# Performance work log

Hardware: AMD Instinct MI355X
Metric: run time of the kernel (lower is better)

## Reference

```python
import jax, jax.numpy as jnp
import numpy as np

V = 128000
SHORTLIST = 10  # cutoffs[0]


def _gru_cell(x, h, w_ih, w_hh, b_ih, b_hh):
    # PyTorch GRU cell math. x: [B, In], h: [B, H], w_*: [3H, *]
    gi = x @ w_ih.T + b_ih  # [B, 3H]
    gh = h @ w_hh.T + b_hh  # [B, 3H]
    i_r, i_z, i_n = jnp.split(gi, 3, axis=-1)
    h_r, h_z, h_n = jnp.split(gh, 3, axis=-1)
    r = jax.nn.sigmoid(i_r + h_r)
    z = jax.nn.sigmoid(i_z + h_z)
    n = jnp.tanh(i_n + r * h_n)
    return (1.0 - z) * n + z * h


def setup_inputs() -> dict:
    key = jax.random.key(0)
    ks = jax.random.split(key, 20)
    B, E, H = 256, 512, 1024
    s = 0.02
    return {
        "input": jax.random.randint(ks[0], (B,), 0, V),
        "hidden": jax.random.normal(ks[1], (2, B, H), jnp.float32),
        "start_state": jnp.zeros((2, B, H), jnp.float32),
        "emb": jax.random.normal(ks[2], (V, E), jnp.float32) * s,
        "w_ih0": jax.random.normal(ks[3], (3 * H, E), jnp.float32) * s,
        "w_hh0": jax.random.normal(ks[4], (3 * H, H), jnp.float32) * s,
        "b_ih0": jax.random.normal(ks[5], (3 * H,), jnp.float32) * s,
        "b_hh0": jax.random.normal(ks[6], (3 * H,), jnp.float32) * s,
        "w_ih1": jax.random.normal(ks[7], (3 * H, H), jnp.float32) * s,
        "w_hh1": jax.random.normal(ks[8], (3 * H, H), jnp.float32) * s,
        "b_ih1": jax.random.normal(ks[9], (3 * H,), jnp.float32) * s,
        "b_hh1": jax.random.normal(ks[10], (3 * H,), jnp.float32) * s,
        "head_w": jax.random.normal(ks[11], (12, H), jnp.float32) * s,
        "t0_proj": jax.random.normal(ks[12], (256, H), jnp.float32) * s,
        "t0_out": jax.random.normal(ks[13], (2, 256), jnp.float32) * s,
        "t1_proj": jax.random.normal(ks[14], (64, H), jnp.float32) * s,
        "t1_out": jax.random.normal(ks[15], (V - 12, 64), jnp.float32) * s,
    }


def reference(input, hidden, start_state, emb, w_ih0, w_hh0, b_ih0, b_hh0,
              w_ih1, w_hh1, b_ih1, b_hh1, head_w, t0_proj, t0_out, t1_proj, t1_out):
    # Embedding lookup (seq_len = 1, squeezed away)
    x = emb[input]  # [B, E]
    # Stacked single-step GRU (eval mode: no dropout)
    h0 = _gru_cell(x, hidden[0], w_ih0, w_hh0, b_ih0, b_hh0)
    h1 = _gru_cell(h0, hidden[1], w_ih1, w_hh1, b_ih1, b_hh1)
    new_hidden = jnp.stack([h0, h1], axis=0)
    out = h1  # [B, H]
    # AdaptiveLogSoftmax.log_prob: head + two tail clusters
    head_lp = jax.nn.log_softmax(out @ head_w.T, axis=-1)  # [B, 12]
    c0 = jax.nn.log_softmax((out @ t0_proj.T) @ t0_out.T, axis=-1)  # [B, 2]
    c1 = jax.nn.log_softmax((out @ t1_proj.T) @ t1_out.T, axis=-1)  # [B, V-12]
    prediction = jnp.concatenate([
        head_lp[:, :SHORTLIST],
        c0 + head_lp[:, SHORTLIST:SHORTLIST + 1],
        c1 + head_lp[:, SHORTLIST + 1:SHORTLIST + 2],
    ], axis=-1)  # [B, V]
    return prediction, new_hidden
```

## Files before the change

kernel.cpp:

```cpp
#include <hip/hip_runtime.h>
#include <hip/hip_bf16.h>
#include <math.h>


#define BM 64
#define BN 64
#define BK 32

typedef __attribute__((ext_vector_type(8))) short frag_ab;
typedef __attribute__((ext_vector_type(4))) float frag_cd;
typedef __attribute__((ext_vector_type(4))) float floatx4;

__device__ __forceinline__ unsigned short f2bf(float f) {
    unsigned int u = __builtin_bit_cast(unsigned int, f);
    u += 0x7fffu + ((u >> 16) & 1u);
    return (unsigned short)(u >> 16);
}

__global__ __launch_bounds__(256) void gru_gemm(const int* __restrict__ idx,
                                                const float* __restrict__ A_ih,
                                                const float* __restrict__ A_hh,
                                                const float* __restrict__ W_ih,
                                                const float* __restrict__ W_hh,
                                                float* __restrict__ outbase,
                                                int Kih, int Khh) {
    const int z = blockIdx.z;
    const int side = z >> 1, half = z & 1;
    const int K = side ? Khh : Kih;
    const int Kh = K >> 1;
    const float* A = side ? A_hh : A_ih;
    const float* W = side ? W_hh : W_ih;
    float* C = outbase + (size_t)z * 786432;

    __shared__ unsigned short As[BM * BK];
    __shared__ unsigned short Wsh[BN * BK];
    const int m0 = blockIdx.y * BM, n0 = blockIdx.x * BN;
    const int t = threadIdx.x;
    const int lane = t & 63, wid = t >> 6;
    const int wm = wid >> 1, wn = wid & 1;
    const int quad = lane >> 4, l16 = lane & 15;
    const int lr = t >> 2;
    const int lc = (t & 3) * 8;

    const int m = m0 + lr;
    const float* arow = (side == 0 && idx) ? A + (size_t)idx[m] * K
                                           : A + (size_t)m * K;
    arow += (size_t)half * Kh + lc;
    const float* wrow = W + (size_t)(n0 + lr) * K + (size_t)half * Kh + lc;

    frag_cd zero4 = {0.f, 0.f, 0.f, 0.f};
    frag_cd acc[2][2] = {{zero4, zero4}, {zero4, zero4}};

    for (int k0 = 0; k0 < Kh; k0 += BK) {
        floatx4 a0 = *(const floatx4*)(arow + k0);
        floatx4 a1 = *(const floatx4*)(arow + k0 + 4);
        floatx4 w0 = *(const floatx4*)(wrow + k0);
        floatx4 w1 = *(const floatx4*)(wrow + k0 + 4);
        frag_ab apk, wpk;
#pragma unroll
        for (int i = 0; i < 4; i++) {
            apk[i]     = (short)f2bf(a0[i]);
            apk[4 + i] = (short)f2bf(a1[i]);
            wpk[i]     = (short)f2bf(w0[i]);
            wpk[4 + i] = (short)f2bf(w1[i]);
        }
        __syncthreads();
        *(frag_ab*)&As[lr * BK + lc] = apk;
        *(frag_ab*)&Wsh[lr * BK + lc] = wpk;
        __syncthreads();

        frag_ab bfr[2];
#pragma unroll
        for (int tn = 0; tn < 2; tn++)
            bfr[tn] = *(const frag_ab*)&Wsh[(wn * 32 + tn * 16 + l16) * BK + quad * 8];
#pragma unroll
        for (int tm = 0; tm < 2; tm++) {
            frag_ab af = *(const frag_ab*)&As[(wm * 32 + tm * 16 + l16) * BK + quad * 8];
#pragma unroll
            for (int tn = 0; tn < 2; tn++)
                acc[tm][tn] = __builtin_amdgcn_mfma_f32_16x16x32_bf16(af, bfr[tn], acc[tm][tn], 0, 0, 0);
        }
    }
#pragma unroll
    for (int tm = 0; tm < 2; tm++)
#pragma unroll
        for (int tn = 0; tn < 2; tn++) {
            int col = n0 + wn * 32 + tn * 16 + l16;
#pragma unroll
            for (int r = 0; r < 4; r++) {
                int row = m0 + wm * 32 + tm * 16 + quad * 4 + r;
                C[(size_t)row * 3072 + col] = acc[tm][tn][r];
            }
        }
}

__global__ __launch_bounds__(256) void gru_gate(const float* __restrict__ P,
                                                const float* __restrict__ b_ih,
                                                const float* __restrict__ b_hh,
                                                const float* __restrict__ hprev,
                                                float* __restrict__ hout) {
    int idx = blockIdx.x * 256 + threadIdx.x;
    int b = idx >> 10, j = idx & 1023;
    const float* g = P + (size_t)b * 3072 + j;
    float ir  = g[0]    + g[786432]        + b_ih[j];
    float iz  = g[1024] + g[786432 + 1024] + b_ih[1024 + j];
    float in_ = g[2048] + g[786432 + 2048] + b_ih[2048 + j];
    const float* gh = g + 2 * 786432;
    float hr  = gh[0]    + gh[786432]        + b_hh[j];
    float hz  = gh[1024] + gh[786432 + 1024] + b_hh[1024 + j];
    float hn  = gh[2048] + gh[786432 + 2048] + b_hh[2048 + j];
    float r = 1.f / (1.f + __expf(-(ir + hr)));
    float z = 1.f / (1.f + __expf(-(iz + hz)));
    float n = tanhf(in_ + r * hn);
    hout[idx] = (1.f - z) * n + z * hprev[idx];
}

__global__ __launch_bounds__(256) void small_gemm(const float* __restrict__ A,
                                                  const float* __restrict__ head_w,
                                                  const float* __restrict__ t0_proj,
                                                  const float* __restrict__ t1_proj,
                                                  float* __restrict__ c_p) {
    const int K = 1024, Kh = 512;
    const int half = blockIdx.z;
    float* C = c_p + (size_t)half * 98304;

    __shared__ unsigned short As[BM * BK];
    __shared__ unsigned short Wsh[BN * BK];
    const int m0 = blockIdx.y * BM, n0 = blockIdx.x * BN;
    const int t = threadIdx.x;
    const int lane = t & 63, wid = t >> 6;
    const int wm = wid >> 1, wn = wid & 1;
    const int quad = lane >> 4, l16 = lane & 15;
    const int lr = t >> 2;
    const int lc = (t & 3) * 8;

    const float* arow = A + (size_t)(m0 + lr) * K + (size_t)half * Kh + lc;
    int wr = n0 + lr;
    const float* wrow;
    if (wr < 12)       wrow = head_w  + (size_t)wr * K;
    else if (wr < 268) wrow = t0_proj + (size_t)(wr - 12) * K;
    else if (wr < 332) wrow = t1_proj + (size_t)(wr - 268) * K;
    else               wrow = nullptr;
    if (wrow) wrow += (size_t)half * Kh + lc;

    frag_cd zero4 = {0.f, 0.f, 0.f, 0.f};
    frag_cd acc[2][2] = {{zero4, zero4}, {zero4, zero4}};

    for (int k0 = 0; k0 < Kh; k0 += BK) {
        floatx4 a0 = *(const floatx4*)(arow + k0);
        floatx4 a1 = *(const floatx4*)(arow + k0 + 4);
        floatx4 w0 = {0.f, 0.f, 0.f, 0.f}, w1 = {0.f, 0.f, 0.f, 0.f};
        if (wrow) {
            w0 = *(const floatx4*)(wrow + k0);
            w1 = *(const floatx4*)(wrow + k0 + 4);
        }
        frag_ab apk, wpk;
#pragma unroll
        for (int i = 0; i < 4; i++) {
            apk[i]     = (short)f2bf(a0[i]);
            apk[4 + i] = (short)f2bf(a1[i]);
            wpk[i]     = (short)f2bf(w0[i]);
            wpk[4 + i] = (short)f2bf(w1[i]);
        }
        __syncthreads();
        *(frag_ab*)&As[lr * BK + lc] = apk;
        *(frag_ab*)&Wsh[lr * BK + lc] = wpk;
        __syncthreads();

        frag_ab bfr[2];
#pragma unroll
        for (int tn = 0; tn < 2; tn++)
            bfr[tn] = *(const frag_ab*)&Wsh[(wn * 32 + tn * 16 + l16) * BK + quad * 8];
#pragma unroll
        for (int tm = 0; tm < 2; tm++) {
            frag_ab af = *(const frag_ab*)&As[(wm * 32 + tm * 16 + l16) * BK + quad * 8];
#pragma unroll
            for (int tn = 0; tn < 2; tn++)
                acc[tm][tn] = __builtin_amdgcn_mfma_f32_16x16x32_bf16(af, bfr[tn], acc[tm][tn], 0, 0, 0);
        }
    }
#pragma unroll
    for (int tm = 0; tm < 2; tm++)
#pragma unroll
        for (int tn = 0; tn < 2; tn++) {
            int col = n0 + wn * 32 + tn * 16 + l16;
#pragma unroll
            for (int r = 0; r < 4; r++) {
                int row = m0 + wm * 32 + tm * 16 + quad * 4 + r;
                C[(size_t)row * 384 + col] = acc[tm][tn][r];
            }
        }
}

__global__ __launch_bounds__(256) void postproc(const float* __restrict__ c_p,
                                                const float* __restrict__ t0_out,
                                                float* __restrict__ outp,
                                                float* __restrict__ abuf,
                                                float* __restrict__ h11buf) {
    int b = blockIdx.x, t = threadIdx.x;
    __shared__ float c[332];
    __shared__ float a0s[4], a1s[4];
    __shared__ float sh_lse;
    for (int j = t; j < 332; j += 256)
        c[j] = c_p[(size_t)b * 384 + j] + c_p[98304 + (size_t)b * 384 + j];
    __syncthreads();
    if (t == 0) {
        float m = c[0];
        for (int i = 1; i < 12; i++) m = fmaxf(m, c[i]);
        float se = 0.f;
        for (int i = 0; i < 12; i++) se += __expf(c[i] - m);
        sh_lse = m + logf(se);
    }
    __syncthreads();
    if (t < 10) outp[(size_t)b * 128000 + t] = c[t] - sh_lse;
    if (t < 64) abuf[(size_t)b * 64 + t] = c[268 + t];

    float pv = c[12 + t];
    float s0 = pv * t0_out[t];
    float s1 = pv * t0_out[256 + t];
    s0 += __shfl_xor(s0, 1);  s0 += __shfl_xor(s0, 2);  s0 += __shfl_xor(s0, 4);
    s0 += __shfl_xor(s0, 8);  s0 += __shfl_xor(s0, 16); s0 += __shfl_xor(s0, 32);
    s1 += __shfl_xor(s1, 1);  s1 += __shfl_xor(s1, 2);  s1 += __shfl_xor(s1, 4);
    s1 += __shfl_xor(s1, 8);  s1 += __shfl_xor(s1, 16); s1 += __shfl_xor(s1, 32);
    if ((t & 63) == 0) { a0s[t >> 6] = s0; a1s[t >> 6] = s1; }
    __syncthreads();
    if (t == 0) {
        float l0 = a0s[0] + a0s[1] + a0s[2] + a0s[3];
        float l1 = a1s[0] + a1s[1] + a1s[2] + a1s[3];
        float m = fmaxf(l0, l1);
        float lse2 = m + logf(__expf(l0 - m) + __expf(l1 - m));
        float hp = c[10] - sh_lse;
        outp[(size_t)b * 128000 + 10] = l0 - lse2 + hp;
        outp[(size_t)b * 128000 + 11] = l1 - lse2 + hp;
        h11buf[b] = c[11] - sh_lse;
    }
}

__global__ __launch_bounds__(256) void big_pass1(const float* __restrict__ A,
                                                 const float* __restrict__ W,
                                                 float* __restrict__ partials) {
    const int N = 127988, K = 64;
    __shared__ unsigned short As[BM * BK];
    __shared__ unsigned short Wsh[BN * BK];
    __shared__ float rowsum[BM];
    const int m0 = blockIdx.y * BM, n0 = blockIdx.x * BN;
    const int t = threadIdx.x;
    const int lane = t & 63, wid = t >> 6;
    const int wm = wid >> 1, wn = wid & 1;
    const int quad = lane >> 4, l16 = lane & 15;
    const int lr = t >> 2;
    const int lc = (t & 3) * 8;

    if (t < BM) rowsum[t] = 0.f;

    const float* arow = A + (size_t)(m0 + lr) * K + lc;
    int wr = n0 + lr;
    const float* wrow = (wr < N) ? W + (size_t)wr * K + lc : nullptr;

    frag_cd zero4 = {0.f, 0.f, 0.f, 0.f};
    frag_cd acc[2][2] = {{zero4, zero4}, {zero4, zero4}};

    for (int k0 = 0; k0 < K; k0 += BK) {
        floatx4 a0 = *(const floatx4*)(arow + k0);
        floatx4 a1 = *(const floatx4*)(arow + k0 + 4);
        floatx4 w0 = {0.f, 0.f, 0.f, 0.f}, w1 = {0.f, 0.f, 0.f, 0.f};
        if (wrow) {
            w0 = *(const floatx4*)(wrow + k0);
            w1 = *(const floatx4*)(wrow + k0 + 4);
        }
        frag_ab apk, wpk;
#pragma unroll
        for (int i = 0; i < 4; i++) {
            apk[i]     = (short)f2bf(a0[i]);
            apk[4 + i] = (short)f2bf(a1[i]);
            wpk[i]     = (short)f2bf(w0[i]);
            wpk[4 + i] = (short)f2bf(w1[i]);
        }
        __syncthreads();
        *(frag_ab*)&As[lr * BK + lc] = apk;
        *(frag_ab*)&Wsh[lr * BK + lc] = wpk;
        __syncthreads();

        frag_ab bfr[2];
#pragma unroll
        for (int tn = 0; tn < 2; tn++)
            bfr[tn] = *(const frag_ab*)&Wsh[(wn * 32 + tn * 16 + l16) * BK + quad * 8];
#pragma unroll
        for (int tm = 0; tm < 2; tm++) {
            frag_ab af = *(const frag_ab*)&As[(wm * 32 + tm * 16 + l16) * BK + quad * 8];
#pragma unroll
            for (int tn = 0; tn < 2; tn++)
                acc[tm][tn] = __builtin_amdgcn_mfma_f32_16x16x32_bf16(af, bfr[tn], acc[tm][tn], 0, 0, 0);
        }
    }

#pragma unroll
    for (int tm = 0; tm < 2; tm++) {
#pragma unroll
        for (int r = 0; r < 4; r++) {
            float s = 0.f;
#pragma unroll
            for (int tn = 0; tn < 2; tn++) {
                int col = n0 + wn * 32 + tn * 16 + l16;
                if (col < N) s += __expf(acc[tm][tn][r]);
            }
            s += __shfl_xor(s, 1);
            s += __shfl_xor(s, 2);
            s += __shfl_xor(s, 4);
            s += __shfl_xor(s, 8);
            if (l16 == 0) atomicAdd(&rowsum[wm * 32 + tm * 16 + quad * 4 + r], s);
        }
    }
    __syncthreads();
    if (t < BM) partials[(size_t)(m0 + t) * 2048 + blockIdx.x] = rowsum[t];
}

__global__ __launch_bounds__(256) void reduce_kernel(const float* __restrict__ partials,
                                                     const float* __restrict__ h11buf,
                                                     float* __restrict__ rowOff) {
    int b = blockIdx.x, t = threadIdx.x;
    __shared__ float a[4];
    float s = 0.f;
    for (int k = t; k < 2000; k += 256) s += partials[(size_t)b * 2048 + k];
    s += __shfl_xor(s, 1);  s += __shfl_xor(s, 2);  s += __shfl_xor(s, 4);
    s += __shfl_xor(s, 8);  s += __shfl_xor(s, 16); s += __shfl_xor(s, 32);
    if ((t & 63) == 0) a[t >> 6] = s;
    __syncthreads();
    if (t == 0) rowOff[b] = h11buf[b] - logf(a[0] + a[1] + a[2] + a[3]);
}

__global__ __launch_bounds__(256) void big_pass2(const float* __restrict__ A,
                                                 const float* __restrict__ W,
                                                 const float* __restrict__ rowOff,
                                                 float* __restrict__ outp) {
    const int N = 127988, K = 64;
    __shared__ unsigned short As[BM * BK];
    __shared__ unsigned short Wsh[BN * BK];
    __shared__ float ro[BM];
    const int m0 = blockIdx.y * BM, n0 = blockIdx.x * BN;
    const int t = threadIdx.x;
    const int lane = t & 63, wid = t >> 6;
    const int wm = wid >> 1, wn = wid & 1;
    const int quad = lane >> 4, l16 = lane & 15;
    const int lr = t >> 2;
    const int lc = (t & 3) * 8;

    if (t < BM) ro[t] = rowOff[m0 + t];

    const float* arow = A + (size_t)(m0 + lr) * K + lc;
    int wr = n0 + lr;
    const float* wrow = (wr < N) ? W + (size_t)wr * K + lc : nullptr;

    frag_cd zero4 = {0.f, 0.f, 0.f, 0.f};
    frag_cd acc[2][2] = {{zero4, zero4}, {zero4, zero4}};

    for (int k0 = 0; k0 < K; k0 += BK) {
        floatx4 a0 = *(const floatx4*)(arow + k0);
        floatx4 a1 = *(const floatx4*)(arow + k0 + 4);
        floatx4 w0 = {0.f, 0.f, 0.f, 0.f}, w1 = {0.f, 0.f, 0.f, 0.f};
        if (wrow) {
            w0 = *(const floatx4*)(wrow + k0);
            w1 = *(const floatx4*)(wrow + k0 + 4);
        }
        frag_ab apk, wpk;
#pragma unroll
        for (int i = 0; i < 4; i++) {
            apk[i]     = (short)f2bf(a0[i]);
            apk[4 + i] = (short)f2bf(a1[i]);
            wpk[i]     = (short)f2bf(w0[i]);
            wpk[4 + i] = (short)f2bf(w1[i]);
        }
        __syncthreads();
        *(frag_ab*)&As[lr * BK + lc] = apk;
        *(frag_ab*)&Wsh[lr * BK + lc] = wpk;
        __syncthreads();

        frag_ab bfr[2];
#pragma unroll
        for (int tn = 0; tn < 2; tn++)
            bfr[tn] = *(const frag_ab*)&Wsh[(wn * 32 + tn * 16 + l16) * BK + quad * 8];
#pragma unroll
        for (int tm = 0; tm < 2; tm++) {
            frag_ab af = *(const frag_ab*)&As[(wm * 32 + tm * 16 + l16) * BK + quad * 8];
#pragma unroll
            for (int tn = 0; tn < 2; tn++)
                acc[tm][tn] = __builtin_amdgcn_mfma_f32_16x16x32_bf16(af, bfr[tn], acc[tm][tn], 0, 0, 0);
        }
    }

#pragma unroll
    for (int tm = 0; tm < 2; tm++)
#pragma unroll
        for (int tn = 0; tn < 2; tn++) {
            int col = n0 + wn * 32 + tn * 16 + l16;
            if (col < N) {
#pragma unroll
                for (int r = 0; r < 4; r++) {
                    int rl = wm * 32 + tm * 16 + quad * 4 + r;
                    outp[(size_t)(m0 + rl) * 128000 + 12 + col] = acc[tm][tn][r] + ro[rl];
                }
            }
        }
}

extern "C" void kernel_launch(void* const* d_in, const int* in_sizes, int n_in,
                              void* d_out, int out_size, void* d_ws, size_t ws_size,
                              hipStream_t stream) {
    const int*   input  = (const int*)d_in[0];
    const float* hidden = (const float*)d_in[1];
    const float* emb    = (const float*)d_in[3];
    const float* w_ih0  = (const float*)d_in[4];
    const float* w_hh0  = (const float*)d_in[5];
    const float* b_ih0  = (const float*)d_in[6];
    const float* b_hh0  = (const float*)d_in[7];
    const float* w_ih1  = (const float*)d_in[8];
    const float* w_hh1  = (const float*)d_in[9];
    const float* b_ih1  = (const float*)d_in[10];
    const float* b_hh1  = (const float*)d_in[11];
    const float* head_w = (const float*)d_in[12];
    const float* t0_proj = (const float*)d_in[13];
    const float* t0_out  = (const float*)d_in[14];
    const float* t1_proj = (const float*)d_in[15];
    const float* t1_out  = (const float*)d_in[16];

    float* outp = (float*)d_out;
    float* ws   = (float*)d_ws;

    float* gruws    = ws;
    float* c_p      = gruws + 4 * 786432;
    float* abuf     = c_p + 2 * 98304;
    float* h11buf   = abuf + 16384;
    float* rowOff   = h11buf + 256;
    float* partials = rowOff + 256;

    float* h0 = outp + 32768000;
    float* h1 = h0 + 262144;

    gru_gemm<<<dim3(48, 4, 4), 256, 0, stream>>>(input, emb, hidden,
                                                 w_ih0, w_hh0, gruws, 512, 1024);
    gru_gate<<<1024, 256, 0, stream>>>(gruws, b_ih0, b_hh0, hidden, h0);
    gru_gemm<<<dim3(48, 4, 4), 256, 0, stream>>>(nullptr, h0, hidden + 262144,
                                                 w_ih1, w_hh1, gruws, 1024, 1024);
    gru_gate<<<1024, 256, 0, stream>>>(gruws, b_ih1, b_hh1, hidden + 262144, h1);
    small_gemm<<<dim3(6, 4, 2), 256, 0, stream>>>(h1, head_w, t0_proj, t1_proj, c_p);
    postproc<<<256, 256, 0, stream>>>(c_p, t0_out, outp, abuf, h11buf);
    big_pass1<<<dim3(2000, 4), 256, 0, stream>>>(abuf, t1_out, partials);
    reduce_kernel<<<256, 256, 0, stream>>>(partials, h11buf, rowOff);
    big_pass2<<<dim3(2000, 4), 256, 0, stream>>>(abuf, t1_out, rowOff, outp);
}
```

Baseline: 519.6 us.

## Pre-convert operands to bf16 and restructure GEMMs to load MFMA fragments directly

New measurement: 577.2 us. 1.11x slower.

```diff
diff --git a/kernel.cpp b/kernel.cpp
--- a/kernel.cpp
+++ b/kernel.cpp
@@ -1,15 +1,11 @@
 #include <hip/hip_runtime.h>
-#include <hip/hip_bf16.h>
 #include <math.h>
 
-
-#define BM 64
-#define BN 64
-#define BK 32
 
 typedef __attribute__((ext_vector_type(8))) short frag_ab;
 typedef __attribute__((ext_vector_type(4))) float frag_cd;
 typedef __attribute__((ext_vector_type(4))) float floatx4;
+typedef __attribute__((ext_vector_type(4))) unsigned short ushortx4;
 
 __device__ __forceinline__ unsigned short f2bf(float f) {
     unsigned int u = __builtin_bit_cast(unsigned int, f);
@@ -17,69 +13,102 @@
     return (unsigned short)(u >> 16);
 }
 
-__global__ __launch_bounds__(256) void gru_gemm(const int* __restrict__ idx,
-                                                const float* __restrict__ A_ih,
-                                                const float* __restrict__ A_hh,
-                                                const float* __restrict__ W_ih,
-                                                const float* __restrict__ W_hh,
+#define XB_OFF      0u
+#define HB0_OFF     131072u
+#define HB1_OFF     393216u
+#define H0B_OFF     655360u
+#define H1B_OFF     917504u
+#define ABUF_OFF    1179648u
+#define WIH0_OFF    1196032u
+#define WHH0_OFF    2768896u
+#define WIH1_OFF    5914624u
+#define WHH1_OFF    9060352u
+#define WSM_OFF     12206080u
+#define WT1_OFF     12599296u
+
+__global__ __launch_bounds__(256) void prep(const int* __restrict__ idx,
+                                            const float* __restrict__ emb,
+                                            const float* __restrict__ hidden,
+                                            const float* __restrict__ w_ih0,
+                                            const float* __restrict__ w_hh0,
+                                            const float* __restrict__ w_ih1,
+                                            const float* __restrict__ w_hh1,
+                                            const float* __restrict__ head_w,
+                                            const float* __restrict__ t0_proj,
+                                            const float* __restrict__ t1_proj,
+                                            unsigned short* __restrict__ dst) {
+    for (int i = blockIdx.x * 256 + threadIdx.x; i < 3014656; i += gridDim.x * 256) {
+        const float* src;
+        unsigned short* d;
+        if (i < 1179648) {
+            if (i < 393216) { src = w_ih0 + (size_t)i * 4; d = dst + WIH0_OFF + (size_t)i * 4; }
+            else { int j = i - 393216; src = w_hh0 + (size_t)j * 4; d = dst + WHH0_OFF + (size_t)j * 4; }
+        } else if (i < 2752512) {
+            if (i < 1966080) { int j = i - 1179648; src = w_ih1 + (size_t)j * 4; d = dst + WIH1_OFF + (size_t)j * 4; }
+            else { int j = i - 1966080; src = w_hh1 + (size_t)j * 4; d = dst + WHH1_OFF + (size_t)j * 4; }
+        } else if (i < 2850816) {
+            int j = i - 2752512;
+            int row = j >> 8, cv = (j & 255) * 4;
+            d = dst + WSM_OFF + (size_t)j * 4;
+            if (row < 12)       src = head_w + (size_t)row * 1024 + cv;
+            else if (row < 268) src = t0_proj + (size_t)(row - 12) * 1024 + cv;
+            else if (row < 332) src = t1_proj + (size_t)(row - 268) * 1024 + cv;
+            else                src = nullptr;
+        } else if (i < 2883584) {
+            int j = i - 2850816;
+            int b = j >> 7, cv = (j & 127) * 4;
+            src = emb + (size_t)idx[b] * 512 + cv;
+            d = dst + XB_OFF + (size_t)j * 4;
+        } else if (i < 2949120) {
+            int j = i - 2883584; src = hidden + (size_t)j * 4; d = dst + HB0_OFF + (size_t)j * 4;
+        } else {
+            int j = i - 2949120; src = hidden + 262144 + (size_t)j * 4; d = dst + HB1_OFF + (size_t)j * 4;
+        }
+        floatx4 v = {0.f, 0.f, 0.f, 0.f};
+        if (src) v = *(const floatx4*)src;
+        ushortx4 o;
+        o[0] = f2bf(v[0]); o[1] = f2bf(v[1]); o[2] = f2bf(v[2]); o[3] = f2bf(v[3]);
+        *(ushortx4*)d = o;
+    }
+}
+
+__global__ __launch_bounds__(256) void gru_gemm(const unsigned short* __restrict__ A_ih,
+                                                const unsigned short* __restrict__ A_hh,
+                                                const unsigned short* __restrict__ W_ih,
+                                                const unsigned short* __restrict__ W_hh,
                                                 float* __restrict__ outbase,
                                                 int Kih, int Khh) {
     const int z = blockIdx.z;
     const int side = z >> 1, half = z & 1;
     const int K = side ? Khh : Kih;
     const int Kh = K >> 1;
-    const float* A = side ? A_hh : A_ih;
-    const float* W = side ? W_hh : W_ih;
+    const unsigned short* A = side ? A_hh : A_ih;
+    const unsigned short* W = side ? W_hh : W_ih;
     float* C = outbase + (size_t)z * 786432;
 
-    __shared__ unsigned short As[BM * BK];
-    __shared__ unsigned short Wsh[BN * BK];
-    const int m0 = blockIdx.y * BM, n0 = blockIdx.x * BN;
+    const int m0 = blockIdx.y * 64, n0 = blockIdx.x * 64;
     const int t = threadIdx.x;
     const int lane = t & 63, wid = t >> 6;
     const int wm = wid >> 1, wn = wid & 1;
     const int quad = lane >> 4, l16 = lane & 15;
-    const int lr = t >> 2;
-    const int lc = (t & 3) * 8;
-
-    const int m = m0 + lr;
-    const float* arow = (side == 0 && idx) ? A + (size_t)idx[m] * K
-                                           : A + (size_t)m * K;
-    arow += (size_t)half * Kh + lc;
-    const float* wrow = W + (size_t)(n0 + lr) * K + (size_t)half * Kh + lc;
+
+    const unsigned short* ap0 = A + (size_t)(m0 + wm * 32 + l16) * K + half * Kh + quad * 8;
+    const unsigned short* ap1 = ap0 + (size_t)16 * K;
+    const unsigned short* bp0 = W + (size_t)(n0 + wn * 32 + l16) * K + half * Kh + quad * 8;
+    const unsigned short* bp1 = bp0 + (size_t)16 * K;
 
     frag_cd zero4 = {0.f, 0.f, 0.f, 0.f};
     frag_cd acc[2][2] = {{zero4, zero4}, {zero4, zero4}};
-
-    for (int k0 = 0; k0 < Kh; k0 += BK) {
-        floatx4 a0 = *(const floatx4*)(arow + k0);
-        floatx4 a1 = *(const floatx4*)(arow + k0 + 4);
-        floatx4 w0 = *(const floatx4*)(wrow + k0);
-        floatx4 w1 = *(const floatx4*)(wrow + k0 + 4);
-        frag_ab apk, wpk;
-#pragma unroll
-        for (int i = 0; i < 4; i++) {
-            apk[i]     = (short)f2bf(a0[i]);
-            apk[4 + i] = (short)f2bf(a1[i]);
-            wpk[i]     = (short)f2bf(w0[i]);
-            wpk[4 + i] = (short)f2bf(w1[i]);
-        }
-        __syncthreads();
-        *(frag_ab*)&As[lr * BK + lc] = apk;
-        *(frag_ab*)&Wsh[lr * BK + lc] = wpk;
-        __syncthreads();
-
-        frag_ab bfr[2];
-#pragma unroll
-        for (int tn = 0; tn < 2; tn++)
-            bfr[tn] = *(const frag_ab*)&Wsh[(wn * 32 + tn * 16 + l16) * BK + quad * 8];
-#pragma unroll
-        for (int tm = 0; tm < 2; tm++) {
-            frag_ab af = *(const frag_ab*)&As[(wm * 32 + tm * 16 + l16) * BK + quad * 8];
-#pragma unroll
-            for (int tn = 0; tn < 2; tn++)
-                acc[tm][tn] = __builtin_amdgcn_mfma_f32_16x16x32_bf16(af, bfr[tn], acc[tm][tn], 0, 0, 0);
-        }
+#pragma unroll 4
+    for (int k0 = 0; k0 < Kh; k0 += 32) {
+        frag_ab a0 = *(const frag_ab*)(ap0 + k0);
+        frag_ab a1 = *(const frag_ab*)(ap1 + k0);
+        frag_ab b0 = *(const frag_ab*)(bp0 + k0);
+        frag_ab b1 = *(const frag_ab*)(bp1 + k0);
+        acc[0][0] = __builtin_amdgcn_mfma_f32_16x16x32_bf16(a0, b0, acc[0][0], 0, 0, 0);
+        acc[0][1] = __builtin_amdgcn_mfma_f32_16x16x32_bf16(a0, b1, acc[0][1], 0, 0, 0);
+        acc[1][0] = __builtin_amdgcn_mfma_f32_16x16x32_bf16(a1, b0, acc[1][0], 0, 0, 0);
+        acc[1][1] = __builtin_amdgcn_mfma_f32_16x16x32_bf16(a1, b1, acc[1][1], 0, 0, 0);
     }
 #pragma unroll
     for (int tm = 0; tm < 2; tm++)
@@ -98,7 +127,8 @@
                                                 const float* __restrict__ b_ih,
                                                 const float* __restrict__ b_hh,
                                                 const float* __restrict__ hprev,
-                                                float* __restrict__ hout) {
+                                                float* __restrict__ hout,
+                                                unsigned short* __restrict__ hb) {
     int idx = blockIdx.x * 256 + threadIdx.x;
     int b = idx >> 10, j = idx & 1023;
     const float* g = P + (size_t)b * 3072 + j;
@@ -112,72 +142,41 @@
     float r = 1.f / (1.f + __expf(-(ir + hr)));
     float z = 1.f / (1.f + __expf(-(iz + hz)));
     float n = tanhf(in_ + r * hn);
-    hout[idx] = (1.f - z) * n + z * hprev[idx];
-}
-
-__global__ __launch_bounds__(256) void small_gemm(const float* __restrict__ A,
-                                                  const float* __restrict__ head_w,
-                                                  const float* __restrict__ t0_proj,
-                                                  const float* __restrict__ t1_proj,
+    float v = (1.f - z) * n + z * hprev[idx];
+    hout[idx] = v;
+    hb[idx] = f2bf(v);
+}
+
+__global__ __launch_bounds__(256) void small_gemm(const unsigned short* __restrict__ A,
+                                                  const unsigned short* __restrict__ Wsm,
                                                   float* __restrict__ c_p) {
     const int K = 1024, Kh = 512;
     const int half = blockIdx.z;
     float* C = c_p + (size_t)half * 98304;
 
-    __shared__ unsigned short As[BM * BK];
-    __shared__ unsigned short Wsh[BN * BK];
-    const int m0 = blockIdx.y * BM, n0 = blockIdx.x * BN;
+    const int m0 = blockIdx.y * 64, n0 = blockIdx.x * 64;
     const int t = threadIdx.x;
     const int lane = t & 63, wid = t >> 6;
     const int wm = wid >> 1, wn = wid & 1;
     const int quad = lane >> 4, l16 = lane & 15;
-    const int lr = t >> 2;
-    const int lc = (t & 3) * 8;
-
-    const float* arow = A + (size_t)(m0 + lr) * K + (size_t)half * Kh + lc;
-    int wr = n0 + lr;
-    const float* wrow;
-    if (wr < 12)       wrow = head_w  + (size_t)wr * K;
-    else if (wr < 268) wrow = t0_proj + (size_t)(wr - 12) * K;
-    else if (wr < 332) wrow = t1_proj + (size_t)(wr - 268) * K;
-    else               wrow = nullptr;
-    if (wrow) wrow += (size_t)half * Kh + lc;
+
+    const unsigned short* ap0 = A + (size_t)(m0 + wm * 32 + l16) * K + half * Kh + quad * 8;
+    const unsigned short* ap1 = ap0 + (size_t)16 * K;
+    const unsigned short* bp0 = Wsm + (size_t)(n0 + wn * 32 + l16) * K + half * Kh + quad * 8;
+    const unsigned short* bp1 = bp0 + (size_t)16 * K;
 
     frag_cd zero4 = {0.f, 0.f, 0.f, 0.f};
     frag_cd acc[2][2] = {{zero4, zero4}, {zero4, zero4}};
-
-    for (int k0 = 0; k0 < Kh; k0 += BK) {
-        floatx4 a0 = *(const floatx4*)(arow + k0);
-        floatx4 a1 = *(const floatx4*)(arow + k0 + 4);
-        floatx4 w0 = {0.f, 0.f, 0.f, 0.f}, w1 = {0.f, 0.f, 0.f, 0.f};
-        if (wrow) {
-            w0 = *(const floatx4*)(wrow + k0);
-            w1 = *(const floatx4*)(wrow + k0 + 4);
-        }
-        frag_ab apk, wpk;
-#pragma unroll
-        for (int i = 0; i < 4; i++) {
-            apk[i]     = (short)f2bf(a0[i]);
-            apk[4 + i] = (short)f2bf(a1[i]);
-            wpk[i]     = (short)f2bf(w0[i]);
-            wpk[4 + i] = (short)f2bf(w1[i]);
-        }
-        __syncthreads();
-        *(frag_ab*)&As[lr * BK + lc] = apk;
-        *(frag_ab*)&Wsh[lr * BK + lc] = wpk;
-        __syncthreads();
-
-        frag_ab bfr[2];
-#pragma unroll
-        for (int tn = 0; tn < 2; tn++)
-            bfr[tn] = *(const frag_ab*)&Wsh[(wn * 32 + tn * 16 + l16) * BK + quad * 8];
-#pragma unroll
-        for (int tm = 0; tm < 2; tm++) {
-            frag_ab af = *(const frag_ab*)&As[(wm * 32 + tm * 16 + l16) * BK + quad * 8];
-#pragma unroll
-            for (int tn = 0; tn < 2; tn++)
-                acc[tm][tn] = __builtin_amdgcn_mfma_f32_16x16x32_bf16(af, bfr[tn], acc[tm][tn], 0, 0, 0);
-        }
+#pragma unroll 4
+    for (int k0 = 0; k0 < Kh; k0 += 32) {
+        frag_ab a0 = *(const frag_ab*)(ap0 + k0);
+        frag_ab a1 = *(const frag_ab*)(ap1 + k0);
+        frag_ab b0 = *(const frag_ab*)(bp0 + k0);
+        frag_ab b1 = *(const frag_ab*)(bp1 + k0);
+        acc[0][0] = __builtin_amdgcn_mfma_f32_16x16x32_bf16(a0, b0, acc[0][0], 0, 0, 0);
+        acc[0][1] = __builtin_amdgcn_mfma_f32_16x16x32_bf16(a0, b1, acc[0][1], 0, 0, 0);
+        acc[1][0] = __builtin_amdgcn_mfma_f32_16x16x32_bf16(a1, b0, acc[1][0], 0, 0, 0);
+        acc[1][1] = __builtin_amdgcn_mfma_f32_16x16x32_bf16(a1, b1, acc[1][1], 0, 0, 0);
     }
 #pragma unroll
     for (int tm = 0; tm < 2; tm++)
@@ -195,7 +194,7 @@
 __global__ __launch_bounds__(256) void postproc(const float* __restrict__ c_p,
                                                 const float* __restrict__ t0_out,
                                                 float* __restrict__ outp,
-                                                float* __restrict__ abuf,
+                                                unsigned short* __restrict__ abuf,
                                                 float* __restrict__ h11buf) {
     int b = blockIdx.x, t = threadIdx.x;
     __shared__ float c[332];
@@ -213,7 +212,7 @@
     }
     __syncthreads();
     if (t < 10) outp[(size_t)b * 128000 + t] = c[t] - sh_lse;
-    if (t < 64) abuf[(size_t)b * 64 + t] = c[268 + t];
+    if (t < 64) abuf[(size_t)b * 64 + t] = f2bf(c[268 + t]);
 
     float pv = c[12 + t];
     float s0 = pv * t0_out[t];
@@ -236,83 +235,72 @@
     }
 }
 
-__global__ __launch_bounds__(256) void big_pass1(const float* __restrict__ A,
+__global__ __launch_bounds__(256) void big_pass1(const unsigned short* __restrict__ Ab,
                                                  const float* __restrict__ W,
+                                                 unsigned short* __restrict__ Wb,
                                                  float* __restrict__ partials) {
-    const int N = 127988, K = 64;
-    __shared__ unsigned short As[BM * BK];
-    __shared__ unsigned short Wsh[BN * BK];
-    __shared__ float rowsum[BM];
-    const int m0 = blockIdx.y * BM, n0 = blockIdx.x * BN;
+    const int N = 127988;
     const int t = threadIdx.x;
     const int lane = t & 63, wid = t >> 6;
-    const int wm = wid >> 1, wn = wid & 1;
     const int quad = lane >> 4, l16 = lane & 15;
-    const int lr = t >> 2;
-    const int lc = (t & 3) * 8;
-
-    if (t < BM) rowsum[t] = 0.f;
-
-    const float* arow = A + (size_t)(m0 + lr) * K + lc;
-    int wr = n0 + lr;
-    const float* wrow = (wr < N) ? W + (size_t)wr * K + lc : nullptr;
-
-    frag_cd zero4 = {0.f, 0.f, 0.f, 0.f};
-    frag_cd acc[2][2] = {{zero4, zero4}, {zero4, zero4}};
-
-    for (int k0 = 0; k0 < K; k0 += BK) {
-        floatx4 a0 = *(const floatx4*)(arow + k0);
-        floatx4 a1 = *(const floatx4*)(arow + k0 + 4);
-        floatx4 w0 = {0.f, 0.f, 0.f, 0.f}, w1 = {0.f, 0.f, 0.f, 0.f};
-        if (wrow) {
-            w0 = *(const floatx4*)(wrow + k0);
-            w1 = *(const floatx4*)(wrow + k0 + 4);
-        }
-        frag_ab apk, wpk;
-#pragma unroll
-        for (int i = 0; i < 4; i++) {
-            apk[i]     = (short)f2bf(a0[i]);
-            apk[4 + i] = (short)f2bf(a1[i]);
-            wpk[i]     = (short)f2bf(w0[i]);
-            wpk[4 + i] = (short)f2bf(w1[i]);
-        }
-        __syncthreads();
-        *(frag_ab*)&As[lr * BK + lc] = apk;
-        *(frag_ab*)&Wsh[lr * BK + lc] = wpk;
-        __syncthreads();
-
-        frag_ab bfr[2];
-#pragma unroll
-        for (int tn = 0; tn < 2; tn++)
-            bfr[tn] = *(const frag_ab*)&Wsh[(wn * 32 + tn * 16 + l16) * BK + quad * 8];
-#pragma unroll
-        for (int tm = 0; tm < 2; tm++) {
-            frag_ab af = *(const frag_ab*)&As[(wm * 32 + tm * 16 + l16) * BK + quad * 8];
-#pragma unroll
-            for (int tn = 0; tn < 2; tn++)
-                acc[tm][tn] = __builtin_amdgcn_mfma_f32_16x16x32_bf16(af, bfr[tn], acc[tm][tn], 0, 0, 0);
-        }
-    }
-
-#pragma unroll
-    for (int tm = 0; tm < 2; tm++) {
+
+    frag_ab a[4][2];
+#pragma unroll
+    for (int mf = 0; mf < 4; mf++)
+#pragma unroll
+        for (int kf = 0; kf < 2; kf++)
+            a[mf][kf] = *(const frag_ab*)(Ab + (size_t)(wid * 64 + mf * 16 + l16) * 64 + kf * 32 + quad * 8);
+
+    float rs[4][4] = {};
+    for (int tt = 0; tt < 4; tt++) {
+        const int n0 = (blockIdx.x * 4 + tt) * 16;
+        const int nr = n0 + l16;
+        frag_ab bw0 = {0, 0, 0, 0, 0, 0, 0, 0};
+        frag_ab bw1 = {0, 0, 0, 0, 0, 0, 0, 0};
+        if (nr < N) {
+            const float* wp = W + (size_t)nr * 64 + quad * 8;
+            floatx4 w0 = *(const floatx4*)wp;
+            floatx4 w1 = *(const floatx4*)(wp + 4);
+            floatx4 w2 = *(const floatx4*)(wp + 32);
+            floatx4 w3 = *(const floatx4*)(wp + 36);
+#pragma unroll
+            for (int i = 0; i < 4; i++) {
+                bw0[i]     = (short)f2bf(w0[i]);
+                bw0[4 + i] = (short)f2bf(w1[i]);
+                bw1[i]     = (short)f2bf(w2[i]);
+                bw1[4 + i] = (short)f2bf(w3[i]);
+            }
+        }
+        if (wid == 0) {
+            unsigned short* wd = Wb + (size_t)nr * 64 + quad * 8;
+            *(frag_ab*)wd = bw0;
+            *(frag_ab*)(wd + 32) = bw1;
+        }
+        frag_cd zero4 = {0.f, 0.f, 0.f, 0.f};
+        frag_cd acc[4] = {zero4, zero4, zero4, zero4};
+#pragma unroll
+        for (int mf = 0; mf < 4; mf++) {
+            acc[mf] = __builtin_amdgcn_mfma_f32_16x16x32_bf16(a[mf][0], bw0, acc[mf], 0, 0, 0);
+            acc[mf] = __builtin_amdgcn_mfma_f32_16x16x32_bf16(a[mf][1], bw1, acc[mf], 0, 0, 0);
+        }
+        if (nr < N) {
+#pragma unroll
+            for (int mf = 0; mf < 4; mf++)
+#pragma unroll
+                for (int r = 0; r < 4; r++)
+                    rs[mf][r] += __expf(acc[mf][r]);
+        }
+    }
+#pragma unroll
+    for (int mf = 0; mf < 4; mf++)
 #pragma unroll
         for (int r = 0; r < 4; r++) {
-            float s = 0.f;
-#pragma unroll
-            for (int tn = 0; tn < 2; tn++) {
-                int col = n0 + wn * 32 + tn * 16 + l16;
-                if (col < N) s += __expf(acc[tm][tn][r]);
-            }
-            s += __shfl_xor(s, 1);
-            s += __shfl_xor(s, 2);
-            s += __shfl_xor(s, 4);
-            s += __shfl_xor(s, 8);
-            if (l16 == 0) atomicAdd(&rowsum[wm * 32 + tm * 16 + quad * 4 + r], s);
-        }
-    }
-    __syncthreads();
-    if (t < BM) partials[(size_t)(m0 + t) * 2048 + blockIdx.x] = rowsum[t];
+            float s = rs[mf][r];
+            s += __shfl_xor(s, 1); s += __shfl_xor(s, 2);
+            s += __shfl_xor(s, 4); s += __shfl_xor(s, 8);
+            if (l16 == 0)
+                partials[(size_t)(wid * 64 + mf * 16 + quad * 4 + r) * 2048 + blockIdx.x] = s;
+        }
 }
 
 __global__ __launch_bounds__(256) void reduce_kernel(const float* __restrict__ partials,
@@ -329,78 +317,51 @@
     if (t == 0) rowOff[b] = h11buf[b] - logf(a[0] + a[1] + a[2] + a[3]);
 }
 
-__global__ __launch_bounds__(256) void big_pass2(const float* __restrict__ A,
-                                                 const float* __restrict__ W,
+__global__ __launch_bounds__(256) void big_pass2(const unsigned short* __restrict__ Ab,
+                                                 const unsigned short* __restrict__ Wb,
                                                  const float* __restrict__ rowOff,
                                                  float* __restrict__ outp) {
-    const int N = 127988, K = 64;
-    __shared__ unsigned short As[BM * BK];
-    __shared__ unsigned short Wsh[BN * BK];
-    __shared__ float ro[BM];
-    const int m0 = blockIdx.y * BM, n0 = blockIdx.x * BN;
+    const int N = 127988;
     const int t = threadIdx.x;
     const int lane = t & 63, wid = t >> 6;
-    const int wm = wid >> 1, wn = wid & 1;
     const int quad = lane >> 4, l16 = lane & 15;
-    const int lr = t >> 2;
-    const int lc = (t & 3) * 8;
-
-    if (t < BM) ro[t] = rowOff[m0 + t];
-
-    const float* arow = A + (size_t)(m0 + lr) * K + lc;
-    int wr = n0 + lr;
-    const float* wrow = (wr < N) ? W + (size_t)wr * K + lc : nullptr;
-
-    frag_cd zero4 = {0.f, 0.f, 0.f, 0.f};
-    frag_cd acc[2][2] = {{zero4, zero4}, {zero4, zero4}};
-
-    for (int k0 = 0; k0 < K; k0 += BK) {
-        floatx4 a0 = *(const floatx4*)(arow + k0);
-        floatx4 a1 = *(const floatx4*)(arow + k0 + 4);
-        floatx4 w0 = {0.f, 0.f, 0.f, 0.f}, w1 = {0.f, 0.f, 0.f, 0.f};
-        if (wrow) {
-            w0 = *(const floatx4*)(wrow + k0);
-            w1 = *(const floatx4*)(wrow + k0 + 4);
-        }
-        frag_ab apk, wpk;
-#pragma unroll
-        for (int i = 0; i < 4; i++) {
-            apk[i]     = (short)f2bf(a0[i]);
-            apk[4 + i] = (short)f2bf(a1[i]);
-            wpk[i]     = (short)f2bf(w0[i]);
-            wpk[4 + i] = (short)f2bf(w1[i]);
-        }
-        __syncthreads();
-        *(frag_ab*)&As[lr * BK + lc] = apk;
-        *(frag_ab*)&Wsh[lr * BK + lc] = wpk;
-        __syncthreads();
-
-        frag_ab bfr[2];
-#pragma unroll
-        for (int tn = 0; tn < 2; tn++)
-            bfr[tn] = *(const frag_ab*)&Wsh[(wn * 32 + tn * 16 + l16) * BK + quad * 8];
-#pragma unroll
-        for (int tm = 0; tm < 2; tm++) {
-            frag_ab af = *(const frag_ab*)&As[(wm * 32 + tm * 16 + l16) * BK + quad * 8];
-#pragma unroll
-            for (int tn = 0; tn < 2; tn++)
-                acc[tm][tn] = __builtin_amdgcn_mfma_f32_16x16x32_bf16(af, bfr[tn], acc[tm][tn], 0, 0, 0);
-        }
-    }
-
-#pragma unroll
-    for (int tm = 0; tm < 2; tm++)
-#pragma unroll
-        for (int tn = 0; tn < 2; tn++) {
-            int col = n0 + wn * 32 + tn * 16 + l16;
-            if (col < N) {
-#pragma unroll
-                for (int r = 0; r < 4; r++) {
-                    int rl = wm * 32 + tm * 16 + quad * 4 + r;
-                    outp[(size_t)(m0 + rl) * 128000 + 12 + col] = acc[tm][tn][r] + ro[rl];
-                }
-            }
-        }
+
+    frag_ab a[4][2];
+#pragma unroll
+    for (int mf = 0; mf < 4; mf++)
+#pragma unroll
+        for (int kf = 0; kf < 2; kf++)
+            a[mf][kf] = *(const frag_ab*)(Ab + (size_t)(wid * 64 + mf * 16 + l16) * 64 + kf * 32 + quad * 8);
+
+    float ro[4][4];
+#pragma unroll
+    for (int mf = 0; mf < 4; mf++)
+#pragma unroll
+        for (int r = 0; r < 4; r++)
+            ro[mf][r] = rowOff[wid * 64 + mf * 16 + quad * 4 + r];
+
+    for (int tt = 0; tt < 4; tt++) {
+        const int n0 = (blockIdx.x * 4 + tt) * 16;
+        const int nr = n0 + l16;
+        const unsigned short* wp = Wb + (size_t)nr * 64 + quad * 8;
+        frag_ab bw0 = *(const frag_ab*)wp;
+        frag_ab bw1 = *(const frag_ab*)(wp + 32);
+        frag_cd zero4 = {0.f, 0.f, 0.f, 0.f};
+        frag_cd acc[4] = {zero4, zero4, zero4, zero4};
+#pragma unroll
+        for (int mf = 0; mf < 4; mf++) {
+            acc[mf] = __builtin_amdgcn_mfma_f32_16x16x32_bf16(a[mf][0], bw0, acc[mf], 0, 0, 0);
+            acc[mf] = __builtin_amdgcn_mfma_f32_16x16x32_bf16(a[mf][1], bw1, acc[mf], 0, 0, 0);
+        }
+        if (nr < N) {
+#pragma unroll
+            for (int mf = 0; mf < 4; mf++)
+#pragma unroll
+                for (int r = 0; r < 4; r++)
+                    outp[(size_t)(wid * 64 + mf * 16 + quad * 4 + r) * 128000 + 12 + nr] =
+                        acc[mf][r] + ro[mf][r];
+        }
+    }
 }
 
 extern "C" void kernel_launch(void* const* d_in, const int* in_sizes, int n_in,
@@ -427,24 +388,37 @@
     float* ws   = (float*)d_ws;
 
     float* gruws    = ws;
-    float* c_p      = gruws + 4 * 786432;
-    float* abuf     = c_p + 2 * 98304;
-    float* h11buf   = abuf + 16384;
+    float* c_p      = gruws + 3145728;
+    float* partials = c_p + 196608;
+    float* h11buf   = partials + 524288;
     float* rowOff   = h11buf + 256;
-    float* partials = rowOff + 256;
+    unsigned short* us = (unsigned short*)(rowOff + 256);
+
+    unsigned short* xb    = us + XB_OFF;
+    unsigned short* hb0   = us + HB0_OFF;
+    unsigned short* hb1   = us + HB1_OFF;
+    unsigned short* h0b   = us + H0B_OFF;
+    unsigned short* h1b   = us + H1B_OFF;
+    unsigned short* abufb = us + ABUF_OFF;
+    unsigned short* wih0  = us + WIH0_OFF;
+    unsigned short* whh0  = us + WHH0_OFF;
+    unsigned short* wih1  = us + WIH1_OFF;
+    unsigned short* whh1  = us + WHH1_OFF;
+    unsigned short* wsm   = us + WSM_OFF;
+    unsigned short* wt1   = us + WT1_OFF;
 
     float* h0 = outp + 32768000;
     float* h1 = h0 + 262144;
 
-    gru_gemm<<<dim3(48, 4, 4), 256, 0, stream>>>(input, emb, hidden,
-                                                 w_ih0, w_hh0, gruws, 512, 1024);
-    gru_gate<<<1024, 256, 0, stream>>>(gruws, b_ih0, b_hh0, hidden, h0);
-    gru_gemm<<<dim3(48, 4, 4), 256, 0, stream>>>(nullptr, h0, hidden + 262144,
-                                                 w_ih1, w_hh1, gruws, 1024, 1024);
-    gru_gate<<<1024, 256, 0, stream>>>(gruws, b_ih1, b_hh1, hidden + 262144, h1);
-    small_gemm<<<dim3(6, 4, 2), 256, 0, stream>>>(h1, head_w, t0_proj, t1_proj, c_p);
-    postproc<<<256, 256, 0, stream>>>(c_p, t0_out, outp, abuf, h11buf);
-    big_pass1<<<dim3(2000, 4), 256, 0, stream>>>(abuf, t1_out, partials);
+    prep<<<2048, 256, 0, stream>>>(input, emb, hidden, w_ih0, w_hh0, w_ih1, w_hh1,
+                                   head_w, t0_proj, t1_proj, us);
+    gru_gemm<<<dim3(48, 4, 4), 256, 0, stream>>>(xb, hb0, wih0, whh0, gruws, 512, 1024);
+    gru_gate<<<1024, 256, 0, stream>>>(gruws, b_ih0, b_hh0, hidden, h0, h0b);
+    gru_gemm<<<dim3(48, 4, 4), 256, 0, stream>>>(h0b, hb1, wih1, whh1, gruws, 1024, 1024);
+    gru_gate<<<1024, 256, 0, stream>>>(gruws, b_ih1, b_hh1, hidden + 262144, h1, h1b);
+    small_gemm<<<dim3(6, 4, 2), 256, 0, stream>>>(h1b, wsm, c_p);
+    postproc<<<256, 256, 0, stream>>>(c_p, t0_out, outp, abufb, h11buf);
+    big_pass1<<<2000, 256, 0, stream>>>(abufb, t1_out, wt1, partials);
     reduce_kernel<<<256, 256, 0, stream>>>(partials, h11buf, rowOff);
-    big_pass2<<<dim3(2000, 4), 256, 0, stream>>>(abuf, t1_out, rowOff, outp);
-}
+    big_pass2<<<2000, 256, 0, stream>>>(abufb, wt1, rowOff, outp);
+}
```

## Double-buffer LDS tiles in GRU GEMMs and stage big_pass2 output through shared memory

Applied to the files above, without the earlier changes.

Result: no change. 516.1 us (-0.7%).

```diff
diff --git a/kernel.cpp b/kernel.cpp
--- a/kernel.cpp
+++ b/kernel.cpp
@@ -1,5 +1,4 @@
 #include <hip/hip_runtime.h>
-#include <hip/hip_bf16.h>
 #include <math.h>
 
 
@@ -32,8 +31,8 @@
     const float* W = side ? W_hh : W_ih;
     float* C = outbase + (size_t)z * 786432;
 
-    __shared__ unsigned short As[BM * BK];
-    __shared__ unsigned short Wsh[BN * BK];
+    __shared__ unsigned short As[2][BM * BK];
+    __shared__ unsigned short Wsh[2][BN * BK];
     const int m0 = blockIdx.y * BM, n0 = blockIdx.x * BN;
     const int t = threadIdx.x;
     const int lane = t & 63, wid = t >> 6;
@@ -51,11 +50,13 @@
     frag_cd zero4 = {0.f, 0.f, 0.f, 0.f};
     frag_cd acc[2][2] = {{zero4, zero4}, {zero4, zero4}};
 
-    for (int k0 = 0; k0 < Kh; k0 += BK) {
-        floatx4 a0 = *(const floatx4*)(arow + k0);
-        floatx4 a1 = *(const floatx4*)(arow + k0 + 4);
-        floatx4 w0 = *(const floatx4*)(wrow + k0);
-        floatx4 w1 = *(const floatx4*)(wrow + k0 + 4);
+    const int nsteps = Kh >> 5;
+
+    floatx4 a0 = *(const floatx4*)(arow);
+    floatx4 a1 = *(const floatx4*)(arow + 4);
+    floatx4 w0 = *(const floatx4*)(wrow);
+    floatx4 w1 = *(const floatx4*)(wrow + 4);
+    {
         frag_ab apk, wpk;
 #pragma unroll
         for (int i = 0; i < 4; i++) {
@@ -64,22 +65,41 @@
             wpk[i]     = (short)f2bf(w0[i]);
             wpk[4 + i] = (short)f2bf(w1[i]);
         }
-        __syncthreads();
-        *(frag_ab*)&As[lr * BK + lc] = apk;
-        *(frag_ab*)&Wsh[lr * BK + lc] = wpk;
-        __syncthreads();
-
-        frag_ab bfr[2];
-#pragma unroll
-        for (int tn = 0; tn < 2; tn++)
-            bfr[tn] = *(const frag_ab*)&Wsh[(wn * 32 + tn * 16 + l16) * BK + quad * 8];
-#pragma unroll
-        for (int tm = 0; tm < 2; tm++) {
-            frag_ab af = *(const frag_ab*)&As[(wm * 32 + tm * 16 + l16) * BK + quad * 8];
-#pragma unroll
-            for (int tn = 0; tn < 2; tn++)
-                acc[tm][tn] = __builtin_amdgcn_mfma_f32_16x16x32_bf16(af, bfr[tn], acc[tm][tn], 0, 0, 0);
-        }
+        *(frag_ab*)&As[0][lr * BK + lc] = apk;
+        *(frag_ab*)&Wsh[0][lr * BK + lc] = wpk;
+    }
+
+    int p = 0;
+    for (int s = 0; s < nsteps; s++) {
+        __syncthreads();
+        if (s + 1 < nsteps) {
+            int k0 = (s + 1) * BK;
+            a0 = *(const floatx4*)(arow + k0);
+            a1 = *(const floatx4*)(arow + k0 + 4);
+            w0 = *(const floatx4*)(wrow + k0);
+            w1 = *(const floatx4*)(wrow + k0 + 4);
+        }
+        frag_ab bfr0 = *(const frag_ab*)&Wsh[p][(wn * 32 + l16) * BK + quad * 8];
+        frag_ab bfr1 = *(const frag_ab*)&Wsh[p][(wn * 32 + 16 + l16) * BK + quad * 8];
+        frag_ab af0  = *(const frag_ab*)&As[p][(wm * 32 + l16) * BK + quad * 8];
+        frag_ab af1  = *(const frag_ab*)&As[p][(wm * 32 + 16 + l16) * BK + quad * 8];
+        acc[0][0] = __builtin_amdgcn_mfma_f32_16x16x32_bf16(af0, bfr0, acc[0][0], 0, 0, 0);
+        acc[0][1] = __builtin_amdgcn_mfma_f32_16x16x32_bf16(af0, bfr1, acc[0][1], 0, 0, 0);
+        acc[1][0] = __builtin_amdgcn_mfma_f32_16x16x32_bf16(af1, bfr0, acc[1][0], 0, 0, 0);
+        acc[1][1] = __builtin_amdgcn_mfma_f32_16x16x32_bf16(af1, bfr1, acc[1][1], 0, 0, 0);
+        if (s + 1 < nsteps) {
+            frag_ab apk, wpk;
+#pragma unroll
+            for (int i = 0; i < 4; i++) {
+                apk[i]     = (short)f2bf(a0[i]);
+                apk[4 + i] = (short)f2bf(a1[i]);
+                wpk[i]     = (short)f2bf(w0[i]);
+                wpk[4 + i] = (short)f2bf(w1[i]);
+            }
+            *(frag_ab*)&As[p ^ 1][lr * BK + lc] = apk;
+            *(frag_ab*)&Wsh[p ^ 1][lr * BK + lc] = wpk;
+        }
+        p ^= 1;
     }
 #pragma unroll
     for (int tm = 0; tm < 2; tm++)
@@ -124,8 +144,8 @@
     const int half = blockIdx.z;
     float* C = c_p + (size_t)half * 98304;
 
-    __shared__ unsigned short As[BM * BK];
-    __shared__ unsigned short Wsh[BN * BK];
+    __shared__ unsigned short As[2][BM * BK];
+    __shared__ unsigned short Wsh[2][BN * BK];
     const int m0 = blockIdx.y * BM, n0 = blockIdx.x * BN;
     const int t = threadIdx.x;
     const int lane = t & 63, wid = t >> 6;
@@ -146,14 +166,16 @@
     frag_cd zero4 = {0.f, 0.f, 0.f, 0.f};
     frag_cd acc[2][2] = {{zero4, zero4}, {zero4, zero4}};
 
-    for (int k0 = 0; k0 < Kh; k0 += BK) {
-        floatx4 a0 = *(const floatx4*)(arow + k0);
-        floatx4 a1 = *(const floatx4*)(arow + k0 + 4);
-        floatx4 w0 = {0.f, 0.f, 0.f, 0.f}, w1 = {0.f, 0.f, 0.f, 0.f};
-        if (wrow) {
-            w0 = *(const floatx4*)(wrow + k0);
-            w1 = *(const floatx4*)(wrow + k0 + 4);
-        }
+    const int nsteps = Kh >> 5;
+
+    floatx4 a0 = *(const floatx4*)(arow);
+    floatx4 a1 = *(const floatx4*)(arow + 4);
+    floatx4 w0 = {0.f, 0.f, 0.f, 0.f}, w1 = {0.f, 0.f, 0.f, 0.f};
+    if (wrow) {
+        w0 = *(const floatx4*)(wrow);
+        w1 = *(const floatx4*)(wrow + 4);
+    }
+    {
         frag_ab apk, wpk;
 #pragma unroll
         for (int i = 0; i < 4; i++) {
@@ -162,22 +184,43 @@
             wpk[i]     = (short)f2bf(w0[i]);
             wpk[4 + i] = (short)f2bf(w1[i]);
         }
-        __syncthreads();
-        *(frag_ab*)&As[lr * BK + lc] = apk;
-        *(frag_ab*)&Wsh[lr * BK + lc] = wpk;
-        __syncthreads();
-
-        frag_ab bfr[2];
-#pragma unroll
-        for (int tn = 0; tn < 2; tn++)
-            bfr[tn] = *(const frag_ab*)&Wsh[(wn * 32 + tn * 16 + l16) * BK + quad * 8];
-#pragma unroll
-        for (int tm = 0; tm < 2; tm++) {
-            frag_ab af = *(const frag_ab*)&As[(wm * 32 + tm * 16 + l16) * BK + quad * 8];
-#pragma unroll
-            for (int tn = 0; tn < 2; tn++)
-                acc[tm][tn] = __builtin_amdgcn_mfma_f32_16x16x32_bf16(af, bfr[tn], acc[tm][tn], 0, 0, 0);
-        }
+        *(frag_ab*)&As[0][lr * BK + lc] = apk;
+        *(frag_ab*)&Wsh[0][lr * BK + lc] = wpk;
+    }
+
+    int p = 0;
+    for (int s = 0; s < nsteps; s++) {
+        __syncthreads();
+        if (s + 1 < nsteps) {
+            int k0 = (s + 1) * BK;
+            a0 = *(const floatx4*)(arow + k0);
+            a1 = *(const floatx4*)(arow + k0 + 4);
+            if (wrow) {
+                w0 = *(const floatx4*)(wrow + k0);
+                w1 = *(const floatx4*)(wrow + k0 + 4);
+            }
+        }
+        frag_ab bfr0 = *(const frag_ab*)&Wsh[p][(wn * 32 + l16) * BK + quad * 8];
+        frag_ab bfr1 = *(const frag_ab*)&Wsh[p][(wn * 32 + 16 + l16) * BK + quad * 8];
+        frag_ab af0  = *(const frag_ab*)&As[p][(wm * 32 + l16) * BK + quad * 8];
+        frag_ab af1  = *(const frag_ab*)&As[p][(wm * 32 + 16 + l16) * BK + quad * 8];
+        acc[0][0] = __builtin_amdgcn_mfma_f32_16x16x32_bf16(af0, bfr0, acc[0][0], 0, 0, 0);
+        acc[0][1] = __builtin_amdgcn_mfma_f32_16x16x32_bf16(af0, bfr1, acc[0][1], 0, 0, 0);
+        acc[1][0] = __builtin_amdgcn_mfma_f32_16x16x32_bf16(af1, bfr0, acc[1][0], 0, 0, 0);
+        acc[1][1] = __builtin_amdgcn_mfma_f32_16x16x32_bf16(af1, bfr1, acc[1][1], 0, 0, 0);
+        if (s + 1 < nsteps) {
+            frag_ab apk, wpk;
+#pragma unroll
+            for (int i = 0; i < 4; i++) {
+                apk[i]     = (short)f2bf(a0[i]);
+                apk[4 + i] = (short)f2bf(a1[i]);
+                wpk[i]     = (short)f2bf(w0[i]);
+                wpk[4 + i] = (short)f2bf(w1[i]);
+            }
+            *(frag_ab*)&As[p ^ 1][lr * BK + lc] = apk;
+            *(frag_ab*)&Wsh[p ^ 1][lr * BK + lc] = wpk;
+        }
+        p ^= 1;
     }
 #pragma unroll
     for (int tm = 0; tm < 2; tm++)
@@ -337,6 +380,7 @@
     __shared__ unsigned short As[BM * BK];
     __shared__ unsigned short Wsh[BN * BK];
     __shared__ float ro[BM];
+    __shared__ float Cs[BM * 68];
     const int m0 = blockIdx.y * BM, n0 = blockIdx.x * BN;
     const int t = threadIdx.x;
     const int lane = t & 63, wid = t >> 6;
@@ -392,15 +436,19 @@
     for (int tm = 0; tm < 2; tm++)
 #pragma unroll
         for (int tn = 0; tn < 2; tn++) {
-            int col = n0 + wn * 32 + tn * 16 + l16;
-            if (col < N) {
-#pragma unroll
-                for (int r = 0; r < 4; r++) {
-                    int rl = wm * 32 + tm * 16 + quad * 4 + r;
-                    outp[(size_t)(m0 + rl) * 128000 + 12 + col] = acc[tm][tn][r] + ro[rl];
-                }
-            }
-        }
+            int col = wn * 32 + tn * 16 + l16;
+#pragma unroll
+            for (int r = 0; r < 4; r++)
+                Cs[(wm * 32 + tm * 16 + quad * 4 + r) * 68 + col] = acc[tm][tn][r];
+        }
+    __syncthreads();
+
+    for (int i = t; i < BM * BN; i += 256) {
+        int rl = i >> 6, col = i & 63;
+        int gc = n0 + col;
+        if (gc < N)
+            outp[(size_t)(m0 + rl) * 128000 + 12 + gc] = Cs[rl * 68 + col] + ro[rl];
+    }
 }
 
 extern "C" void kernel_launch(void* const* d_in, const int* in_sizes, int n_in,
```
